# Performance work log

Measured on AMD Instinct MI355X. Metric: run time of the kernel, lower is better.

Reference implementation:

```python
import jax, jax.numpy as jnp
import numpy as np

DIM = 4096
N_HEADS_Q = 32
N_HEADS_KV = 8
HEAD_DIM = DIM // N_HEADS_Q  # 128
N_REP = N_HEADS_Q // N_HEADS_KV  # 4
HIDDEN = 11008
MAX_BS = 32
MAX_SEQ = 2048
BATCH = 32
SEQ = 1
START_POS = 1024
NORM_EPS = 1e-5


def setup_inputs() -> dict:
    key = jax.random.key(0)
    ks = jax.random.split(key, 10)
    x = jax.random.normal(ks[0], (BATCH, SEQ, DIM), dtype=jnp.float32)
    # RoPE frequencies for positions [START_POS, START_POS+SEQ)
    inv_freq = 1.0 / (10000.0 ** (np.arange(0, HEAD_DIM, 2, dtype=np.float32) / HEAD_DIM))  # [64]
    pos = np.arange(START_POS, START_POS + SEQ, dtype=np.float32)
    angles = pos[:, None] * inv_freq[None, :]  # [SEQ, 64]
    freqs_cos = jnp.asarray(np.cos(angles), dtype=jnp.float32)
    freqs_sin = jnp.asarray(np.sin(angles), dtype=jnp.float32)
    cache_k = jax.random.normal(ks[1], (MAX_BS, MAX_SEQ, N_HEADS_KV, HEAD_DIM), dtype=jnp.float32) * 0.5
    cache_v = jax.random.normal(ks[2], (MAX_BS, MAX_SEQ, N_HEADS_KV, HEAD_DIM), dtype=jnp.float32) * 0.5
    s = 1.0 / np.sqrt(DIM)
    wq = jax.random.normal(ks[3], (DIM, N_HEADS_Q * HEAD_DIM), dtype=jnp.float32) * s
    wk = jax.random.normal(ks[4], (DIM, N_HEADS_KV * HEAD_DIM), dtype=jnp.float32) * s
    wv = jax.random.normal(ks[5], (DIM, N_HEADS_KV * HEAD_DIM), dtype=jnp.float32) * s
    wo = jax.random.normal(ks[6], (DIM, DIM), dtype=jnp.float32) * s
    w1 = jax.random.normal(ks[7], (DIM, HIDDEN), dtype=jnp.float32) * s
    w3 = jax.random.normal(ks[8], (DIM, HIDDEN), dtype=jnp.float32) * s
    w2 = jax.random.normal(ks[9], (HIDDEN, DIM), dtype=jnp.float32) * (1.0 / np.sqrt(HIDDEN))
    attn_norm_w = jnp.ones((DIM,), dtype=jnp.float32)
    ffn_norm_w = jnp.ones((DIM,), dtype=jnp.float32)
    return {"x": x, "start_pos": STAT if False else START_POS, "freqs_cos": freqs_cos, "freqs_sin": freqs_sin,
            "cache_k": cache_k, "cache_v": cache_v, "wq": wq, "wk": wk, "wv": wv, "wo": wo,
            "w1": w1, "w2": w2, "w3": w3, "attn_norm_w": attn_norm_w, "ffn_norm_w": ffn_norm_w}


def _rmsnorm(x, w, eps=NORM_EPS):
    # NOTE: source adds eps AFTER sqrt: x / (sqrt(mean(x^2)) + eps)
    return w * (x / (jnp.sqrt(jnp.mean(x * x, axis=-1, keepdims=True)) + eps))


def _apply_rope(x, cos, sin):
    # x: [B,S,H,D]; cos/sin: [S,D/2] -> complex rotation on interleaved pairs
    B, S, H, D = x.shape
    xr = x.reshape(B, S, H, D // 2, 2)
    x0, x1 = xr[..., 0], xr[..., 1]
    c = cos[None, :, None, :]
    s = sin[None, :, None, :]
    o0 = x0 * c - x1 * s
    o1 = x0 * s + x1 * c
    return jnp.stack([o0, o1], axis=-1).reshape(B, S, H, D)


def reference(x, start_pos, freqs_cos, freqs_sin, cache_k, cache_v,
              wq, wk, wv, wo, w1, w2, w3, attn_norm_w, ffn_norm_w):
    B, S, _ = x.shape
    residue = x
    h = _rmsnorm(x, attn_norm_w)
    q = (h @ wq).reshape(B, S, N_HEADS_Q, HEAD_DIM)
    k = (h @ wk).reshape(B, S, N_HEADS_KV, HEAD_DIM)
    v = (h @ wv).reshape(B, S, N_HEADS_KV, HEAD_DIM)
    q = _apply_rope(q, freqs_cos, freqs_sin)
    k = _apply_rope(k, freqs_cos, freqs_sin)
    # write into KV cache, then read positions [0, start_pos+S)
    cache_k = jax.lax.dynamic_update_slice(cache_k, k, (0, start_pos, 0, 0))
    cache_v = jax.lax.dynamic_update_slice(cache_v, v, (0, start_pos, 0, 0))
    L = start_pos + S
    keys = cache_k[:B, :L]    # [B,L,Hkv,D]
    values = cache_v[:B, :L]  # [B,L,Hkv,D]
    # GQA attention without materializing repeated KV heads
    qg = q.reshape(B, S, N_HEADS_KV, N_REP, HEAD_DIM)
    scores = jnp.einsum('bsgrd,blgd->bgrsl', qg, keys) / jnp.sqrt(jnp.float32(HEAD_DIM))
    attn = jax.nn.softmax(scores, axis=-1)
    out = jnp.einsum('bgrsl,blgd->bsgrd', attn, values).reshape(B, S, N_HEADS_Q * HEAD_DIM)
    out = out @ wo + residue
    residue = out
    h2 = _rmsnorm(out, ffn_norm_w)
    ffn = (jax.nn.silu(h2 @ w1) * (h2 @ w3)) @ w2
    return ffn + residue
```

## Files before the change

### kernel.cpp

```cpp
#include <hip/hip_runtime.h>
#include <math.h>

#define DIM 4096
#define HIDDEN 11008
#define NB 32
#define EPS 1e-5f

__global__ __launch_bounds__(256) void rmsnorm_t_kernel(
    const float* __restrict__ x, const float* __restrict__ w,
    float* __restrict__ outT)
{
  int m = blockIdx.x;
  int tid = threadIdx.x;
  const float4* xr = (const float4*)(x + (size_t)m * DIM);
  const float4* wr = (const float4*)w;
  float4 xv[4];
  float s = 0.f;
#pragma unroll
  for (int i = 0; i < 4; i++) {
    xv[i] = xr[tid + i * 256];
    s += xv[i].x * xv[i].x + xv[i].y * xv[i].y + xv[i].z * xv[i].z + xv[i].w * xv[i].w;
  }
#pragma unroll
  for (int off = 32; off > 0; off >>= 1) s += __shfl_down(s, off, 64);
  __shared__ float wsum[4];
  if ((tid & 63) == 0) wsum[tid >> 6] = s;
  __syncthreads();
  float tot = wsum[0] + wsum[1] + wsum[2] + wsum[3];
  float scale = 1.0f / (sqrtf(tot / (float)DIM) + EPS);
#pragma unroll
  for (int i = 0; i < 4; i++) {
    float4 wv = wr[tid + i * 256];
    int k = (tid + i * 256) * 4;
    outT[(size_t)(k + 0) * NB + m] = xv[i].x * wv.x * scale;
    outT[(size_t)(k + 1) * NB + m] = xv[i].y * wv.y * scale;
    outT[(size_t)(k + 2) * NB + m] = xv[i].z * wv.z * scale;
    outT[(size_t)(k + 3) * NB + m] = xv[i].w * wv.w * scale;
  }
}

__global__ __launch_bounds__(256) void gemm32_kernel(
    const float* __restrict__ AT,
    const float* __restrict__ W,
    float* __restrict__ C,
    int ldw, int ldc, int colOff, int K, int kPerBlk)
{
  __shared__ float Wl[64 * 64];
  __shared__ float Al[64 * 32];
  int tid = threadIdx.x;
  int tn = tid & 63, tm = tid >> 6;
  int colBase = blockIdx.x * 64;
  int k0 = blockIdx.y * kPerBlk;
  int kEnd = k0 + kPerBlk; if (kEnd > K) kEnd = K;
  float acc[8] = {0.f, 0.f, 0.f, 0.f, 0.f, 0.f, 0.f, 0.f};

  for (int kt = k0; kt < kEnd; kt += 64) {
    int tk = kEnd - kt; if (tk > 64) tk = 64;
    __syncthreads();
#pragma unroll
    for (int i = 0; i < 4; i++) {
      int e = tid + i * 256;
      int row = e >> 4, c = (e & 15) << 2;
      float4 v = make_float4(0.f, 0.f, 0.f, 0.f);
      if (row < tk) v = *(const float4*)&W[(size_t)(kt + row) * ldw + colBase + c];
      *(float4*)&Wl[row * 64 + c] = v;
    }
#pragma unroll
    for (int i = 0; i < 2; i++) {
      int e = tid + i * 256;
      int row = e >> 3, c = (e & 7) << 2;
      float4 v = make_float4(0.f, 0.f, 0.f, 0.f);
      if (row < tk) v = *(const float4*)&AT[(size_t)(kt + row) * NB + c];
      *(float4*)&Al[row * NB + c] = v;
    }
    __syncthreads();
#pragma unroll 4
    for (int kk = 0; kk < tk; kk++) {
      float wv = Wl[kk * 64 + tn];
      float4 a0 = *(const float4*)&Al[kk * NB + tm * 8];
      float4 a1 = *(const float4*)&Al[kk * NB + tm * 8 + 4];
      acc[0] += a0.x * wv; acc[1] += a0.y * wv; acc[2] += a0.z * wv; acc[3] += a0.w * wv;
      acc[4] += a1.x * wv; acc[5] += a1.y * wv; acc[6] += a1.z * wv; acc[7] += a1.w * wv;
    }
  }
  float* cb = C + (size_t)(tm * 8) * ldc + colOff + colBase + tn;
#pragma unroll
  for (int i = 0; i < 8; i++) atomicAdd(cb + (size_t)i * ldc, acc[i]);
}

__global__ __launch_bounds__(256) void rope_kernel(
    float* __restrict__ qkv, const float* __restrict__ cosv, const float* __restrict__ sinv)
{
  int idx = blockIdx.x * 256 + threadIdx.x;
  int j = idx & 63;
  int h = (idx >> 6) % 40;
  int b = idx / (64 * 40);
  int col = (h < 32) ? (h * 128 + 2 * j) : (DIM + (h - 32) * 128 + 2 * j);
  float* p = qkv + (size_t)b * 6144 + col;
  float c = cosv[j], s = sinv[j];
  float x0 = p[0], x1 = p[1];
  p[0] = x0 * c - x1 * s;
  p[1] = x0 * s + x1 * c;
}

__global__ __launch_bounds__(256) void attn_kernel(
    const float* __restrict__ qkv,
    const float* __restrict__ ck, const float* __restrict__ cv,
    float* __restrict__ attnoT)
{
  __shared__ float qs[4 * 128];
  __shared__ float sc[4 * 1026];
  __shared__ float kvt[64 * 129];
  __shared__ float invs[4];
  int tid = threadIdx.x;
  int b = blockIdx.x >> 3, g = blockIdx.x & 7;
  const float scale = 0.08838834764831845f;

  for (int i = tid; i < 512; i += 256)
    qs[i] = qkv[(size_t)b * 6144 + (size_t)g * 512 + i];

  const float* kbase = ck + (((size_t)b * 2048) * 8 + g) * 128;
  float4 pre[8];

#pragma unroll
  for (int i = 0; i < 8; i++) {
    int e = tid + i * 256;
    int row = e >> 5, c = (e & 31) << 2;
    pre[i] = *(const float4*)&kbase[(size_t)row * 1024 + c];
  }
#pragma unroll
  for (int i = 0; i < 8; i++) {
    int e = tid + i * 256;
    int row = e >> 5, c = (e & 31) << 2;
    float* d = &kvt[row * 129 + c];
    d[0] = pre[i].x; d[1] = pre[i].y; d[2] = pre[i].z; d[3] = pre[i].w;
  }
  __syncthreads();

  int r1 = tid >> 6, l1 = tid & 63;
  for (int t = 0; t < 16; t++) {
    if (t < 15) {
      int l0 = (t + 1) * 64;
#pragma unroll
      for (int i = 0; i < 8; i++) {
        int e = tid + i * 256;
        int row = e >> 5, c = (e & 31) << 2;
        pre[i] = *(const float4*)&kbase[(size_t)(l0 + row) * 1024 + c];
      }
    }
    float a = 0.f;
    const float* kr = &kvt[l1 * 129];
    const float* qr = &qs[r1 * 128];
#pragma unroll 8
    for (int d = 0; d < 128; d++) a += qr[d] * kr[d];
    sc[r1 * 1026 + t * 64 + l1] = a * scale;
    __syncthreads();
    if (t < 15) {
#pragma unroll
      for (int i = 0; i < 8; i++) {
        int e = tid + i * 256;
        int row = e >> 5, c = (e & 31) << 2;
        float* d = &kvt[row * 129 + c];
        d[0] = pre[i].x; d[1] = pre[i].y; d[2] = pre[i].z; d[3] = pre[i].w;
      }
      __syncthreads();
    }
  }

  {
    const float* kn = qkv + (size_t)b * 6144 + DIM + (size_t)g * 128;
    float part = qs[r1 * 128 + l1] * kn[l1] + qs[r1 * 128 + 64 + l1] * kn[64 + l1];
#pragma unroll
    for (int off = 32; off > 0; off >>= 1) part += __shfl_down(part, off, 64);
    if (l1 == 0) sc[r1 * 1026 + 1024] = part * scale;
  }
  __syncthreads();

  {
    float m = -1e30f;
    for (int l = l1; l < 1025; l += 64) m = fmaxf(m, sc[r1 * 1026 + l]);
#pragma unroll
    for (int off = 32; off > 0; off >>= 1) m = fmaxf(m, __shfl_xor(m, off, 64));
    float ssum = 0.f;
    for (int l = l1; l < 1025; l += 64) {
      float e = __expf(sc[r1 * 1026 + l] - m);
      sc[r1 * 1026 + l] = e;
      ssum += e;
    }
#pragma unroll
    for (int off = 32; off > 0; off >>= 1) ssum += __shfl_xor(ssum, off, 64);
    if (l1 == 0) invs[r1] = 1.0f / ssum;
  }
  __syncthreads();

  const float* vbase = cv + (((size_t)b * 2048) * 8 + g) * 128;
#pragma unroll
  for (int i = 0; i < 8; i++) {
    int e = tid + i * 256;
    int row = e >> 5, c = (e & 31) << 2;
    pre[i] = *(const float4*)&vbase[(size_t)row * 1024 + c];
  }
#pragma unroll
  for (int i = 0; i < 8; i++) {
    int e = tid + i * 256;
    int row = e >> 5, c = (e & 31) << 2;
    float* d = &kvt[row * 129 + c];
    d[0] = pre[i].x; d[1] = pre[i].y; d[2] = pre[i].z; d[3] = pre[i].w;
  }
  __syncthreads();

  int dd = tid & 127, rr = tid >> 7;
  float a0 = 0.f, a1 = 0.f;
  for (int t = 0; t < 16; t++) {
    if (t < 15) {
      int l0 = (t + 1) * 64;
#pragma unroll
      for (int i = 0; i < 8; i++) {
        int e = tid + i * 256;
        int row = e >> 5, c = (e & 31) << 2;
        pre[i] = *(const float4*)&vbase[(size_t)(l0 + row) * 1024 + c];
      }
    }
    const float* p0 = &sc[rr * 1026 + t * 64];
    const float* p1 = &sc[(rr + 2) * 1026 + t * 64];
#pragma unroll 8
    for (int l = 0; l < 64; l++) {
      float v = kvt[l * 129 + dd];
      a0 += p0[l] * v;
      a1 += p1[l] * v;
    }
    __syncthreads();
    if (t < 15) {
#pragma unroll
      for (int i = 0; i < 8; i++) {
        int e = tid + i * 256;
        int row = e >> 5, c = (e & 31) << 2;
        float* d = &kvt[row * 129 + c];
        d[0] = pre[i].x; d[1] = pre[i].y; d[2] = pre[i].z; d[3] = pre[i].w;
      }
      __syncthreads();
    }
  }
  {
    const float* vn = qkv + (size_t)b * 6144 + DIM + 1024 + (size_t)g * 128;
    float v = vn[dd];
    a0 += sc[rr * 1026 + 1024] * v;
    a1 += sc[(rr + 2) * 1026 + 1024] * v;
  }
  float i0 = invs[rr], i1 = invs[rr + 2];
  attnoT[(size_t)((g * 4 + rr) * 128 + dd) * NB + b] = a0 * i0;
  attnoT[(size_t)((g * 4 + rr + 2) * 128 + dd) * NB + b] = a1 * i1;
}

__global__ __launch_bounds__(256) void silu_kernel(
    const float* __restrict__ gu, float* __restrict__ actT)
{
  int idx = blockIdx.x * 256 + threadIdx.x;
  int j = idx >> 5, m = idx & 31;
  float g = gu[(size_t)m * 22016 + j];
  float u = gu[(size_t)m * 22016 + HIDDEN + j];
  float sg = g / (1.0f + __expf(-g));
  actT[idx] = sg * u;
}

__global__ __launch_bounds__(256) void copy4_kernel(
    float* __restrict__ dst, const float* __restrict__ src)
{
  int idx = blockIdx.x * 256 + threadIdx.x;
  ((float4*)dst)[idx] = ((const float4*)src)[idx];
}

extern "C" void kernel_launch(void* const* d_in, const int* in_sizes, int n_in,
                              void* d_out, int out_size, void* d_ws, size_t ws_size,
                              hipStream_t stream)
{
  const float* x   = (const float*)d_in[0];
  const float* fc  = (const float*)d_in[2];
  const float* fs  = (const float*)d_in[3];
  const float* ck  = (const float*)d_in[4];
  const float* cv  = (const float*)d_in[5];
  const float* wq  = (const float*)d_in[6];
  const float* wk  = (const float*)d_in[7];
  const float* wv  = (const float*)d_in[8];
  const float* wo  = (const float*)d_in[9];
  const float* w1  = (const float*)d_in[10];
  const float* w2  = (const float*)d_in[11];
  const float* w3  = (const float*)d_in[12];
  const float* anw = (const float*)d_in[13];
  const float* fnw = (const float*)d_in[14];
  float* out = (float*)d_out;

  float* ws     = (float*)d_ws;
  float* qkv    = ws;
  float* gateup = ws + 196608;
  float* hT     = ws + 901120;
  float* out1   = ws + 1032192;
  float* h2T    = ws + 1163264;
  float* actT   = ws + 1294336;
  float* attnoT = ws + 1646592;

  hipMemsetAsync(qkv, 0, (size_t)(196608 + 704512) * sizeof(float), stream);

  rmsnorm_t_kernel<<<32, 256, 0, stream>>>(x, anw, hT);

  gemm32_kernel<<<dim3(64, 8),  256, 0, stream>>>(hT, wq, qkv, 4096, 6144, 0,    4096, 512);
  gemm32_kernel<<<dim3(16, 32), 256, 0, stream>>>(hT, wk, qkv, 1024, 6144, 4096, 4096, 128);
  gemm32_kernel<<<dim3(16, 32), 256, 0, stream>>>(hT, wv, qkv, 1024, 6144, 5120, 4096, 128);

  rope_kernel<<<320, 256, 0, stream>>>(qkv, fc, fs);

  attn_kernel<<<256, 256, 0, stream>>>(qkv, ck, cv, attnoT);

  copy4_kernel<<<128, 256, 0, stream>>>(out1, x);
  gemm32_kernel<<<dim3(64, 8), 256, 0, stream>>>(attnoT, wo, out1, 4096, 4096, 0, 4096, 512);

  rmsnorm_t_kernel<<<32, 256, 0, stream>>>(out1, fnw, h2T);

  gemm32_kernel<<<dim3(172, 4), 256, 0, stream>>>(h2T, w1, gateup, HIDDEN, 22016, 0,      4096, 1024);
  gemm32_kernel<<<dim3(172, 4), 256, 0, stream>>>(h2T, w3, gateup, HIDDEN, 22016, HIDDEN, 4096, 1024);

  silu_kernel<<<1376, 256, 0, stream>>>(gateup, actT);

  copy4_kernel<<<128, 256, 0, stream>>>(out, out1);
  gemm32_kernel<<<dim3(64, 16), 256, 0, stream>>>(actT, w2, out, 4096, 4096, 0, HIDDEN, 688);
}
```

Baseline: 1.189 ms.

## Replace LDS-tiled skinny GEMM with register-streamed weight GEMM and merge paired launches

The shared-memory tiled GEMM becomes a kernel where each thread streams a float2 column pair of weights from global memory. Loads are double-buffered in registers, and the 32 activation rows are read directly through the cache into 64 per-thread accumulators. The K/V and W1/W3 projections are merged into single launches using blockIdx.z, and split-K factors are retuned. The attention kernel switches to float4 shared-memory accesses with padded strides. The aim is to cut LDS traffic and syncs in this bandwidth-bound decode layer, at the cost of high register pressure and more atomic adds.

Measured after the change: 1.811 ms. 1.52x slower.

```diff
diff --git a/kernel.cpp b/kernel.cpp
--- a/kernel.cpp
+++ b/kernel.cpp
@@ -39,53 +39,70 @@
   }
 }
 
-__global__ __launch_bounds__(256) void gemm32_kernel(
+__global__ __launch_bounds__(256) void gemm32s_kernel(
     const float* __restrict__ AT,
-    const float* __restrict__ W,
-    float* __restrict__ C,
-    int ldw, int ldc, int colOff, int K, int kPerBlk)
-{
-  __shared__ float Wl[64 * 64];
-  __shared__ float Al[64 * 32];
+    const float* __restrict__ W0, const float* __restrict__ W1,
+    float* __restrict__ C, int ldw, int ldc, int colOff0, int colOff1,
+    int K, int kPerBlk)
+{
+  const float* W = blockIdx.z ? W1 : W0;
+  int colOff = blockIdx.z ? colOff1 : colOff0;
   int tid = threadIdx.x;
-  int tn = tid & 63, tm = tid >> 6;
-  int colBase = blockIdx.x * 64;
+  int col = blockIdx.x * 512 + tid * 2;
+  bool active = (col < ldw);
   int k0 = blockIdx.y * kPerBlk;
   int kEnd = k0 + kPerBlk; if (kEnd > K) kEnd = K;
-  float acc[8] = {0.f, 0.f, 0.f, 0.f, 0.f, 0.f, 0.f, 0.f};
-
-  for (int kt = k0; kt < kEnd; kt += 64) {
-    int tk = kEnd - kt; if (tk > 64) tk = 64;
-    __syncthreads();
-#pragma unroll
-    for (int i = 0; i < 4; i++) {
-      int e = tid + i * 256;
-      int row = e >> 4, c = (e & 15) << 2;
-      float4 v = make_float4(0.f, 0.f, 0.f, 0.f);
-      if (row < tk) v = *(const float4*)&W[(size_t)(kt + row) * ldw + colBase + c];
-      *(float4*)&Wl[row * 64 + c] = v;
-    }
-#pragma unroll
-    for (int i = 0; i < 2; i++) {
-      int e = tid + i * 256;
-      int row = e >> 3, c = (e & 7) << 2;
-      float4 v = make_float4(0.f, 0.f, 0.f, 0.f);
-      if (row < tk) v = *(const float4*)&AT[(size_t)(kt + row) * NB + c];
-      *(float4*)&Al[row * NB + c] = v;
-    }
-    __syncthreads();
-#pragma unroll 4
-    for (int kk = 0; kk < tk; kk++) {
-      float wv = Wl[kk * 64 + tn];
-      float4 a0 = *(const float4*)&Al[kk * NB + tm * 8];
-      float4 a1 = *(const float4*)&Al[kk * NB + tm * 8 + 4];
-      acc[0] += a0.x * wv; acc[1] += a0.y * wv; acc[2] += a0.z * wv; acc[3] += a0.w * wv;
-      acc[4] += a1.x * wv; acc[5] += a1.y * wv; acc[6] += a1.z * wv; acc[7] += a1.w * wv;
-    }
-  }
-  float* cb = C + (size_t)(tm * 8) * ldc + colOff + colBase + tn;
-#pragma unroll
-  for (int i = 0; i < 8; i++) atomicAdd(cb + (size_t)i * ldc, acc[i]);
+
+  float acc0[32], acc1[32];
+#pragma unroll
+  for (int r = 0; r < 32; r++) { acc0[r] = 0.f; acc1[r] = 0.f; }
+
+  float2 bufA[8], bufB[8];
+
+#define LOADW(buf, kb)                                                        \
+  {                                                                           \
+    _Pragma("unroll")                                                         \
+    for (int u = 0; u < 8; u++) {                                             \
+      int kk = (kb) + u;                                                      \
+      buf[u] = (active && kk < kEnd)                                          \
+                   ? *(const float2*)&W[(size_t)kk * ldw + col]               \
+                   : make_float2(0.f, 0.f);                                   \
+    }                                                                         \
+  }
+
+#define COMP(buf, kb)                                                         \
+  {                                                                           \
+    _Pragma("unroll")                                                         \
+    for (int u = 0; u < 8; u++) {                                             \
+      int kk = (kb) + u; if (kk > K - 1) kk = K - 1;                          \
+      const float* ar = AT + (size_t)kk * NB;                                 \
+      _Pragma("unroll")                                                       \
+      for (int r = 0; r < 32; r++) {                                          \
+        float a = ar[r];                                                      \
+        acc0[r] += a * buf[u].x;                                              \
+        acc1[r] += a * buf[u].y;                                              \
+      }                                                                       \
+    }                                                                         \
+  }
+
+  LOADW(bufA, k0);
+  for (int k = k0; k < kEnd; k += 16) {
+    LOADW(bufB, k + 8);
+    COMP(bufA, k);
+    LOADW(bufA, k + 16);
+    COMP(bufB, k + 8);
+  }
+#undef LOADW
+#undef COMP
+
+  if (active) {
+    float* cb = C + colOff + col;
+#pragma unroll
+    for (int r = 0; r < 32; r++) {
+      atomicAdd(cb + (size_t)r * ldc,     acc0[r]);
+      atomicAdd(cb + (size_t)r * ldc + 1, acc1[r]);
+    }
+  }
 }
 
 __global__ __launch_bounds__(256) void rope_kernel(
@@ -103,14 +120,16 @@
   p[1] = x0 * s + x1 * c;
 }
 
+#define KVP 132
+#define SCP 1028
 __global__ __launch_bounds__(256) void attn_kernel(
     const float* __restrict__ qkv,
     const float* __restrict__ ck, const float* __restrict__ cv,
     float* __restrict__ attnoT)
 {
   __shared__ float qs[4 * 128];
-  __shared__ float sc[4 * 1026];
-  __shared__ float kvt[64 * 129];
+  __shared__ float sc[4 * SCP];
+  __shared__ float kvt[64 * KVP];
   __shared__ float invs[4];
   int tid = threadIdx.x;
   int b = blockIdx.x >> 3, g = blockIdx.x & 7;
@@ -132,8 +151,7 @@
   for (int i = 0; i < 8; i++) {
     int e = tid + i * 256;
     int row = e >> 5, c = (e & 31) << 2;
-    float* d = &kvt[row * 129 + c];
-    d[0] = pre[i].x; d[1] = pre[i].y; d[2] = pre[i].z; d[3] = pre[i].w;
+    *(float4*)&kvt[row * KVP + c] = pre[i];
   }
   __syncthreads();
 
@@ -149,19 +167,21 @@
       }
     }
     float a = 0.f;
-    const float* kr = &kvt[l1 * 129];
-    const float* qr = &qs[r1 * 128];
-#pragma unroll 8
-    for (int d = 0; d < 128; d++) a += qr[d] * kr[d];
-    sc[r1 * 1026 + t * 64 + l1] = a * scale;
+    const float4* kr = (const float4*)&kvt[l1 * KVP];
+    const float4* qr = (const float4*)&qs[r1 * 128];
+#pragma unroll
+    for (int d = 0; d < 32; d++) {
+      float4 kv = kr[d], qv = qr[d];
+      a += qv.x * kv.x + qv.y * kv.y + qv.z * kv.z + qv.w * kv.w;
+    }
+    sc[r1 * SCP + t * 64 + l1] = a * scale;
     __syncthreads();
     if (t < 15) {
 #pragma unroll
       for (int i = 0; i < 8; i++) {
         int e = tid + i * 256;
         int row = e >> 5, c = (e & 31) << 2;
-        float* d = &kvt[row * 129 + c];
-        d[0] = pre[i].x; d[1] = pre[i].y; d[2] = pre[i].z; d[3] = pre[i].w;
+        *(float4*)&kvt[row * KVP + c] = pre[i];
       }
       __syncthreads();
     }
@@ -172,19 +192,19 @@
     float part = qs[r1 * 128 + l1] * kn[l1] + qs[r1 * 128 + 64 + l1] * kn[64 + l1];
 #pragma unroll
     for (int off = 32; off > 0; off >>= 1) part += __shfl_down(part, off, 64);
-    if (l1 == 0) sc[r1 * 1026 + 1024] = part * scale;
+    if (l1 == 0) sc[r1 * SCP + 1024] = part * scale;
   }
   __syncthreads();
 
   {
     float m = -1e30f;
-    for (int l = l1; l < 1025; l += 64) m = fmaxf(m, sc[r1 * 1026 + l]);
+    for (int l = l1; l < 1025; l += 64) m = fmaxf(m, sc[r1 * SCP + l]);
 #pragma unroll
     for (int off = 32; off > 0; off >>= 1) m = fmaxf(m, __shfl_xor(m, off, 64));
     float ssum = 0.f;
     for (int l = l1; l < 1025; l += 64) {
-      float e = __expf(sc[r1 * 1026 + l] - m);
-      sc[r1 * 1026 + l] = e;
+      float e = __expf(sc[r1 * SCP + l] - m);
+      sc[r1 * SCP + l] = e;
       ssum += e;
     }
 #pragma unroll
@@ -204,8 +224,7 @@
   for (int i = 0; i < 8; i++) {
     int e = tid + i * 256;
     int row = e >> 5, c = (e & 31) << 2;
-    float* d = &kvt[row * 129 + c];
-    d[0] = pre[i].x; d[1] = pre[i].y; d[2] = pre[i].z; d[3] = pre[i].w;
+    *(float4*)&kvt[row * KVP + c] = pre[i];
   }
   __syncthreads();
 
@@ -221,13 +240,18 @@
         pre[i] = *(const float4*)&vbase[(size_t)(l0 + row) * 1024 + c];
       }
     }
-    const float* p0 = &sc[rr * 1026 + t * 64];
-    const float* p1 = &sc[(rr + 2) * 1026 + t * 64];
-#pragma unroll 8
-    for (int l = 0; l < 64; l++) {
-      float v = kvt[l * 129 + dd];
-      a0 += p0[l] * v;
-      a1 += p1[l] * v;
+    const float4* p0 = (const float4*)&sc[rr * SCP + t * 64];
+    const float4* p1 = (const float4*)&sc[(rr + 2) * SCP + t * 64];
+#pragma unroll
+    for (int l4 = 0; l4 < 16; l4++) {
+      float4 q0 = p0[l4], q1 = p1[l4];
+      int lb = l4 * 4;
+      float v0 = kvt[(lb + 0) * KVP + dd];
+      float v1 = kvt[(lb + 1) * KVP + dd];
+      float v2 = kvt[(lb + 2) * KVP + dd];
+      float v3 = kvt[(lb + 3) * KVP + dd];
+      a0 += q0.x * v0 + q0.y * v1 + q0.z * v2 + q0.w * v3;
+      a1 += q1.x * v0 + q1.y * v1 + q1.z * v2 + q1.w * v3;
     }
     __syncthreads();
     if (t < 15) {
@@ -235,8 +259,7 @@
       for (int i = 0; i < 8; i++) {
         int e = tid + i * 256;
         int row = e >> 5, c = (e & 31) << 2;
-        float* d = &kvt[row * 129 + c];
-        d[0] = pre[i].x; d[1] = pre[i].y; d[2] = pre[i].z; d[3] = pre[i].w;
+        *(float4*)&kvt[row * KVP + c] = pre[i];
       }
       __syncthreads();
     }
@@ -244,8 +267,8 @@
   {
     const float* vn = qkv + (size_t)b * 6144 + DIM + 1024 + (size_t)g * 128;
     float v = vn[dd];
-    a0 += sc[rr * 1026 + 1024] * v;
-    a1 += sc[(rr + 2) * 1026 + 1024] * v;
+    a0 += sc[rr * SCP + 1024] * v;
+    a1 += sc[(rr + 2) * SCP + 1024] * v;
   }
   float i0 = invs[rr], i1 = invs[rr + 2];
   attnoT[(size_t)((g * 4 + rr) * 128 + dd) * NB + b] = a0 * i0;
@@ -303,24 +326,22 @@
 
   rmsnorm_t_kernel<<<32, 256, 0, stream>>>(x, anw, hT);
 
-  gemm32_kernel<<<dim3(64, 8),  256, 0, stream>>>(hT, wq, qkv, 4096, 6144, 0,    4096, 512);
-  gemm32_kernel<<<dim3(16, 32), 256, 0, stream>>>(hT, wk, qkv, 1024, 6144, 4096, 4096, 128);
-  gemm32_kernel<<<dim3(16, 32), 256, 0, stream>>>(hT, wv, qkv, 1024, 6144, 5120, 4096, 128);
+  gemm32s_kernel<<<dim3(8, 32, 1), 256, 0, stream>>>(hT, wq, wq, qkv, 4096, 6144, 0, 0, 4096, 128);
+  gemm32s_kernel<<<dim3(2, 64, 2), 256, 0, stream>>>(hT, wk, wv, qkv, 1024, 6144, 4096, 5120, 4096, 64);
 
   rope_kernel<<<320, 256, 0, stream>>>(qkv, fc, fs);
 
   attn_kernel<<<256, 256, 0, stream>>>(qkv, ck, cv, attnoT);
 
   copy4_kernel<<<128, 256, 0, stream>>>(out1, x);
-  gemm32_kernel<<<dim3(64, 8), 256, 0, stream>>>(attnoT, wo, out1, 4096, 4096, 0, 4096, 512);
+  gemm32s_kernel<<<dim3(8, 32, 1), 256, 0, stream>>>(attnoT, wo, wo, out1, 4096, 4096, 0, 0, 4096, 128);
 
   rmsnorm_t_kernel<<<32, 256, 0, stream>>>(out1, fnw, h2T);
 
-  gemm32_kernel<<<dim3(172, 4), 256, 0, stream>>>(h2T, w1, gateup, HIDDEN, 22016, 0,      4096, 1024);
-  gemm32_kernel<<<dim3(172, 4), 256, 0, stream>>>(h2T, w3, gateup, HIDDEN, 22016, HIDDEN, 4096, 1024);
+  gemm32s_kernel<<<dim3(22, 8, 2), 256, 0, stream>>>(h2T, w1, w3, gateup, 11008, 22016, 0, 11008, 4096, 512);
 
   silu_kernel<<<1376, 256, 0, stream>>>(gateup, actT);
 
   copy4_kernel<<<128, 256, 0, stream>>>(out, out1);
-  gemm32_kernel<<<dim3(64, 16), 256, 0, stream>>>(actT, w2, out, 4096, 4096, 0, HIDDEN, 688);
-}
+  gemm32s_kernel<<<dim3(8, 32, 1), 256, 0, stream>>>(actT, w2, w2, out, 4096, 4096, 0, 0, 11008, 344);
+}
```
